# Kernel optimization log

Measured on AMD Instinct MI355X. Metric: run time of the kernel, lower is better.

Reference implementation:

```python
import jax, jax.numpy as jnp
import numpy as np

B, T, VT, E, D = 128, 512, 2048, 1024, 1024  # batch, num_topics, topic_vocab, enc_hid, dec_hid


def setup_inputs() -> dict:
    key = jax.random.key(0)
    ks = jax.random.split(key, 8)
    # Split the Linear weight (in = dec_hid + topic_vocab + enc_hid, concat order: hidden, topic, enc)
    # into per-input blocks; math is identical to Linear(cat([h, t, e])).
    s = 1.0 / np.sqrt(D + VT + E)
    return {
        "hidden": jax.random.normal(ks[0], (B, D), jnp.float32),
        "topic_dict": jax.random.uniform(ks[1], (T, VT), jnp.float32),
        "enc_hidden": jax.random.normal(ks[2], (B, E), jnp.float32),
        "W_h": jax.random.uniform(ks[3], (D, D), jnp.float32, -s, s),
        "W_t": jax.random.uniform(ks[4], (VT, D), jnp.float32, -s, s),
        "W_e": jax.random.uniform(ks[5], (E, D), jnp.float32, -s, s),
        "b": jax.random.uniform(ks[6], (D,), jnp.float32, -s, s),
        "v": jax.random.uniform(ks[7], (D,), jnp.float32),
    }


def reference(hidden, topic_dict, enc_hidden, W_h, W_t, W_e, b, v):
    # Decompose Linear(cat(h, t, e)) = h@W_h + t@W_t + e@W_e + b; avoids the
    # repeated/concatenated [B, T, D+VT+E] buffer while computing the same math.
    h_proj = hidden @ W_h          # [B, D]
    t_proj = topic_dict @ W_t      # [T, D]
    e_proj = enc_hidden @ W_e      # [B, D]
    energy = jnp.tanh(h_proj[:, None, :] + e_proj[:, None, :] + t_proj[None, :, :] + b)  # [B, T, D]
    score = jnp.einsum("btd,d->bt", energy, v)  # [B, T]
    return jax.nn.softmax(score, axis=1)[:, None, :]  # [B, 1, T]
```

## Files before the change

### kernel.cpp

```cpp
#include <hip/hip_runtime.h>
#include <hip/hip_fp16.h>

#define B_ 128
#define T_ 512
#define VT_ 2048
#define E_ 1024
#define D_ 1024

typedef _Float16 h8 __attribute__((ext_vector_type(8)));
typedef float f4 __attribute__((ext_vector_type(4)));

#define C2LE 2.8853900817779268f
#define L2E  1.4426950408889634f

static __device__ __forceinline__ float rcpf(float x) { return __builtin_amdgcn_rcpf(x); }
static __device__ __forceinline__ float ex2(float x)  { return __builtin_amdgcn_exp2f(x); }

#define P_FLOATS   (4 * 640 * 1024)
#define SP_FLOATS  (8 * 128 * 512)
#define PA_HALVES  (640 * 2048)
#define PB_WH      0
#define PB_WE      1048576
#define PB_WT      2097152

__device__ __forceinline__ void packA_do(const float* __restrict__ src, int ld, int KBs,
                                         _Float16* __restrict__ dst, int mb_off, int kb_off, int t)
{
    const int lane = t & 63;
    const int fb = t >> 6;
    const int kb = fb % KBs, mb = fb / KBs;
    const int r = lane & 15, g = lane >> 4;
    const float* s = src + (size_t)(mb * 16 + r) * ld + kb * 32 + g * 8;
    f4 v0 = *(const f4*)s, v1 = *(const f4*)(s + 4);
    h8 h;
    h[0] = (_Float16)v0[0]; h[1] = (_Float16)v0[1]; h[2] = (_Float16)v0[2]; h[3] = (_Float16)v0[3];
    h[4] = (_Float16)v1[0]; h[5] = (_Float16)v1[1]; h[6] = (_Float16)v1[2]; h[7] = (_Float16)v1[3];
    *(h8*)(dst + ((size_t)((mb_off + mb) * 64 + (kb_off + kb)) * 64 + lane) * 8) = h;
}

__device__ __forceinline__ void packB_do(const float* __restrict__ W, int KB,
                                         _Float16* __restrict__ dst, int t)
{
    const int lane = t & 63;
    const int fb = t >> 6;
    const int kb = fb % KB, nb = fb / KB;
    const int r = lane & 15, g = lane >> 4;
    const float* s = W + (size_t)(kb * 32 + g * 8) * 1024 + nb * 16 + r;
    h8 h;
    #pragma unroll
    for (int j = 0; j < 8; ++j) h[j] = (_Float16)s[(size_t)j * 1024];
    *(h8*)(dst + ((size_t)(nb * KB + kb) * 64 + lane) * 8) = h;
}

__global__ __launch_bounds__(256) void pack_kernel(
    const float* __restrict__ hidden, const float* __restrict__ topic,
    const float* __restrict__ enc,
    const float* __restrict__ W_h, const float* __restrict__ W_t, const float* __restrict__ W_e,
    _Float16* __restrict__ pA, _Float16* __restrict__ pB)
{
    const int bid = blockIdx.x, tid = threadIdx.x;
    if      (bid <   64) packA_do(hidden, 1024, 32, pA, 0,  0, bid * 256 + tid);
    else if (bid <  128) packA_do(enc,    1024, 32, pA, 0, 32, (bid -  64) * 256 + tid);
    else if (bid <  640) packA_do(topic,  2048, 64, pA, 8,  0, (bid - 128) * 256 + tid);
    else if (bid < 1152) packB_do(W_h, 32, pB + PB_WH, (bid -  640) * 256 + tid);
    else if (bid < 1664) packB_do(W_e, 32, pB + PB_WE, (bid - 1152) * 256 + tid);
    else                 packB_do(W_t, 64, pB + PB_WT, (bid - 1664) * 256 + tid);
}

__global__ __launch_bounds__(256) void gemm_kernel(const _Float16* __restrict__ pA,
                                                   const _Float16* __restrict__ pB,
                                                   float* __restrict__ P)
{
    const int mt = blockIdx.x, nt = blockIdx.y, s = blockIdx.z;
    const int tid = threadIdx.x, wave = tid >> 6, lane = tid & 63;
    const int wm = (wave >> 1) * 32, wn = (wave & 1) * 32;
    const int r = lane & 15, g = lane >> 4;

    const int kb0 = s * 16;
    const int mb0 = (mt * 64 + wm) >> 4;
    const int nb0 = (nt * 64 + wn) >> 4;

    const _Float16* Bp; int KB_B, kbB;
    if (mt < 2) {
        if (kb0 < 32) { Bp = pB + PB_WH; kbB = kb0; }
        else          { Bp = pB + PB_WE; kbB = kb0 - 32; }
        KB_B = 32;
    } else {
        Bp = pB + PB_WT; kbB = kb0; KB_B = 64;
    }

    const _Float16* Ap = pA + ((size_t)(mb0 * 64 + kb0) * 64 + lane) * 8;
    const _Float16* Bq = Bp + ((size_t)(nb0 * KB_B + kbB) * 64 + lane) * 8;
    const size_t aStrI = (size_t)64 * 512;
    const size_t bStrJ = (size_t)KB_B * 512;

    f4 acc00{}, acc01{}, acc10{}, acc11{};
    #pragma unroll 4
    for (int ks = 0; ks < 16; ++ks) {
        h8 a0 = *(const h8*)(Ap);
        h8 a1 = *(const h8*)(Ap + aStrI);
        h8 b0 = *(const h8*)(Bq);
        h8 b1 = *(const h8*)(Bq + bStrJ);
        acc00 = __builtin_amdgcn_mfma_f32_16x16x32_f16(a0, b0, acc00, 0, 0, 0);
        acc01 = __builtin_amdgcn_mfma_f32_16x16x32_f16(a0, b1, acc01, 0, 0, 0);
        acc10 = __builtin_amdgcn_mfma_f32_16x16x32_f16(a1, b0, acc10, 0, 0, 0);
        acc11 = __builtin_amdgcn_mfma_f32_16x16x32_f16(a1, b1, acc11, 0, 0, 0);
        Ap += 512; Bq += 512;
    }

    float* Pp = P + ((size_t)s * 640 + mt * 64 + wm + g * 4) * 1024 + nt * 64 + wn + r;
    #pragma unroll
    for (int q = 0; q < 4; ++q) {
        Pp[(size_t)q * 1024 +  0]        = C2LE * acc00[q];
        Pp[(size_t)q * 1024 + 16]        = C2LE * acc01[q];
        Pp[(size_t)(16 + q) * 1024 +  0] = C2LE * acc10[q];
        Pp[(size_t)(16 + q) * 1024 + 16] = C2LE * acc11[q];
    }
}

__global__ __launch_bounds__(256) void score_kernel(const float* __restrict__ P,
                                                    const float* __restrict__ bias,
                                                    const float* __restrict__ v,
                                                    float* __restrict__ SP)
{
    __shared__ float Xs[16][128];
    __shared__ float Ys[64][128];
    __shared__ float vs[128];

    const int tid = threadIdx.x;
    const int b0 = blockIdx.x * 16;
    const int t0 = blockIdx.y * 64;
    const int d0 = blockIdx.z * 128;
    const size_t PS = (size_t)640 * 1024;

    #pragma unroll
    for (int i = 0; i < 8; ++i) {
        int idx = tid + i * 256;
        int row = idx >> 5, c4 = idx & 31;
        size_t off = (size_t)(128 + t0 + row) * 1024 + d0 + c4 * 4;
        f4 vv = *(const f4*)&P[off];
        vv += *(const f4*)&P[off + PS];
        vv += *(const f4*)&P[off + 2 * PS];
        vv += *(const f4*)&P[off + 3 * PS];
        *(f4*)&Ys[row][(c4 ^ (row & 15)) * 4] = vv;
    }
    #pragma unroll
    for (int i = 0; i < 2; ++i) {
        int idx = tid + i * 256;
        int row = idx >> 5, c4 = idx & 31;
        size_t off = (size_t)(b0 + row) * 1024 + d0 + c4 * 4;
        f4 vv = *(const f4*)&P[off];
        vv += *(const f4*)&P[off + PS];
        vv += *(const f4*)&P[off + 2 * PS];
        vv += *(const f4*)&P[off + 3 * PS];
        f4 bb = *(const f4*)&bias[d0 + c4 * 4];
        vv += bb * C2LE;
        *(f4*)&Xs[row][(c4 ^ (row & 15)) * 4] = vv;
    }
    if (tid < 32) *(f4*)&vs[tid * 4] = *(const f4*)&v[d0 + tid * 4];
    __syncthreads();

    const int tq = tid & 31, bq = tid >> 5;
    const int sx0 = bq & 15, sx1 = (bq + 8) & 15, sy = tq & 15;
    float a00 = 0.f, a01 = 0.f, a10 = 0.f, a11 = 0.f;

    for (int dd = 0; dd < 32; ++dd) {
        f4 xa = *(const f4*)&Xs[bq]     [(dd ^ sx0) * 4];
        f4 xb = *(const f4*)&Xs[bq + 8] [(dd ^ sx1) * 4];
        f4 ya = *(const f4*)&Ys[tq]     [(dd ^ sy) * 4];
        f4 yb = *(const f4*)&Ys[tq + 32][(dd ^ sy) * 4];
        f4 vv = *(const f4*)&vs[dd * 4];
        #pragma unroll
        for (int j = 0; j < 4; ++j) {
            float e;
            e = ex2(xa[j] + ya[j]); a00 += vv[j] * rcpf(e + 1.0f);
            e = ex2(xa[j] + yb[j]); a01 += vv[j] * rcpf(e + 1.0f);
            e = ex2(xb[j] + ya[j]); a10 += vv[j] * rcpf(e + 1.0f);
            e = ex2(xb[j] + yb[j]); a11 += vv[j] * rcpf(e + 1.0f);
        }
    }

    float* sp = SP + (size_t)blockIdx.z * (B_ * T_);
    sp[(size_t)(b0 + bq)     * T_ + t0 + tq]      = a00;
    sp[(size_t)(b0 + bq)     * T_ + t0 + tq + 32] = a01;
    sp[(size_t)(b0 + bq + 8) * T_ + t0 + tq]      = a10;
    sp[(size_t)(b0 + bq + 8) * T_ + t0 + tq + 32] = a11;
}

__global__ __launch_bounds__(256) void softmax_kernel(
    const float* __restrict__ SP, float* __restrict__ out)
{
    const int b = blockIdx.x, tid = threadIdx.x;
    float s0 = 0.f, s1 = 0.f;
    #pragma unroll
    for (int z = 0; z < 8; ++z) {
        s0 += SP[(size_t)z * B_ * T_ + (size_t)b * T_ + tid];
        s1 += SP[(size_t)z * B_ * T_ + (size_t)b * T_ + tid + 256];
    }
    s0 *= -2.0f; s1 *= -2.0f;

    float m = fmaxf(s0, s1);
    #pragma unroll
    for (int off = 32; off >= 1; off >>= 1) m = fmaxf(m, __shfl_xor(m, off));
    __shared__ float red[4];
    __shared__ float red2[4];
    const int wv = tid >> 6;
    if ((tid & 63) == 0) red[wv] = m;
    __syncthreads();
    m = fmaxf(fmaxf(red[0], red[1]), fmaxf(red[2], red[3]));

    float e0 = ex2((s0 - m) * L2E);
    float e1 = ex2((s1 - m) * L2E);
    float sum = e0 + e1;
    #pragma unroll
    for (int off = 32; off >= 1; off >>= 1) sum += __shfl_xor(sum, off);
    if ((tid & 63) == 0) red2[wv] = sum;
    __syncthreads();
    sum = red2[0] + red2[1] + red2[2] + red2[3];

    const float rs = rcpf(sum);
    out[(size_t)b * T_ + tid]       = e0 * rs;
    out[(size_t)b * T_ + tid + 256] = e1 * rs;
}

extern "C" void kernel_launch(void* const* d_in, const int* in_sizes, int n_in,
                              void* d_out, int out_size, void* d_ws, size_t ws_size,
                              hipStream_t stream)
{
    const float* hidden = (const float*)d_in[0];
    const float* topic  = (const float*)d_in[1];
    const float* enc    = (const float*)d_in[2];
    const float* W_h    = (const float*)d_in[3];
    const float* W_t    = (const float*)d_in[4];
    const float* W_e    = (const float*)d_in[5];
    const float* bvec   = (const float*)d_in[6];
    const float* vvec   = (const float*)d_in[7];
    float* out = (float*)d_out;

    float* P      = (float*)d_ws;
    float* SPb    = P + P_FLOATS;
    _Float16* pA  = (_Float16*)(SPb + SP_FLOATS);
    _Float16* pB  = pA + PA_HALVES;

    pack_kernel<<<2688, 256, 0, stream>>>(hidden, topic, enc, W_h, W_t, W_e, pA, pB);
    gemm_kernel<<<dim3(10, 16, 4), 256, 0, stream>>>(pA, pB, P);
    score_kernel<<<dim3(8, 8, 8), 256, 0, stream>>>(P, bvec, vvec, SPb);
    softmax_kernel<<<128, 256, 0, stream>>>(SPb, out);
}
```

Before: 119.6 us.

## Widen GEMM N-tile, double split-K, add separate partial-sum reduce kernel

The GEMM tile grows from 64x64 to 64x128 per block (each wave computes a 32x64 block with 8 MFMA accumulators), split-K goes from 4 to 8 slices, and a swizzled 1D grid of 640 blocks is used. A new reduce kernel sums the 8 partial slices and adds the bias once, so the score kernel reads a single reduced buffer instead of re-summing partials in every block. This is meant to raise operand reuse and parallelism and to remove redundant partial-sum reads in the score stage. The cost is an extra kernel launch and twice as much partial-sum traffic written and read through memory.

Result: faster. 115.0 us (-3.8%).

```diff
diff --git a/kernel.cpp b/kernel.cpp
--- a/kernel.cpp
+++ b/kernel.cpp
@@ -16,7 +16,8 @@
 static __device__ __forceinline__ float rcpf(float x) { return __builtin_amdgcn_rcpf(x); }
 static __device__ __forceinline__ float ex2(float x)  { return __builtin_amdgcn_exp2f(x); }
 
-#define P_FLOATS   (4 * 640 * 1024)
+#define P_FLOATS   (8 * 640 * 1024)
+#define R_FLOATS   (640 * 1024)
 #define SP_FLOATS  (8 * 128 * 512)
 #define PA_HALVES  (640 * 2048)
 #define PB_WH      0
@@ -67,59 +68,85 @@
     else                 packB_do(W_t, 64, pB + PB_WT, (bid - 1664) * 256 + tid);
 }
 
-__global__ __launch_bounds__(256) void gemm_kernel(const _Float16* __restrict__ pA,
-                                                   const _Float16* __restrict__ pB,
-                                                   float* __restrict__ P)
-{
-    const int mt = blockIdx.x, nt = blockIdx.y, s = blockIdx.z;
+__global__ __launch_bounds__(256, 3) void gemm_kernel(const _Float16* __restrict__ pA,
+                                                      const _Float16* __restrict__ pB,
+                                                      float* __restrict__ P)
+{
+    const int lin = blockIdx.x;
+    const int sw  = (lin & 7) * 80 + (lin >> 3);
+    const int s   = sw / 80;
+    const int rem = sw % 80;
+    const int mt  = rem % 10;
+    const int nt  = rem / 10;
+
     const int tid = threadIdx.x, wave = tid >> 6, lane = tid & 63;
-    const int wm = (wave >> 1) * 32, wn = (wave & 1) * 32;
+    const int wm = (wave >> 1) * 32;
+    const int wn = (wave & 1) * 64;
     const int r = lane & 15, g = lane >> 4;
 
-    const int kb0 = s * 16;
-    const int mb0 = (mt * 64 + wm) >> 4;
-    const int nb0 = (nt * 64 + wn) >> 4;
-
-    const _Float16* Bp; int KB_B, kbB;
+    const int mb0 = mt * 4 + (wm >> 4);
+    const int nb0 = (nt * 128 + wn) >> 4;
+    const int kb0 = s * 8;
+
+    const _Float16* Bp; int KB_B, kbB0;
     if (mt < 2) {
-        if (kb0 < 32) { Bp = pB + PB_WH; kbB = kb0; }
-        else          { Bp = pB + PB_WE; kbB = kb0 - 32; }
+        if (kb0 < 32) { Bp = pB + PB_WH; kbB0 = kb0; }
+        else          { Bp = pB + PB_WE; kbB0 = kb0 - 32; }
         KB_B = 32;
-    } else {
-        Bp = pB + PB_WT; kbB = kb0; KB_B = 64;
-    }
+    } else { Bp = pB + PB_WT; kbB0 = kb0; KB_B = 64; }
 
     const _Float16* Ap = pA + ((size_t)(mb0 * 64 + kb0) * 64 + lane) * 8;
-    const _Float16* Bq = Bp + ((size_t)(nb0 * KB_B + kbB) * 64 + lane) * 8;
-    const size_t aStrI = (size_t)64 * 512;
-    const size_t bStrJ = (size_t)KB_B * 512;
-
-    f4 acc00{}, acc01{}, acc10{}, acc11{};
-    #pragma unroll 4
-    for (int ks = 0; ks < 16; ++ks) {
-        h8 a0 = *(const h8*)(Ap);
-        h8 a1 = *(const h8*)(Ap + aStrI);
-        h8 b0 = *(const h8*)(Bq);
-        h8 b1 = *(const h8*)(Bq + bStrJ);
-        acc00 = __builtin_amdgcn_mfma_f32_16x16x32_f16(a0, b0, acc00, 0, 0, 0);
-        acc01 = __builtin_amdgcn_mfma_f32_16x16x32_f16(a0, b1, acc01, 0, 0, 0);
-        acc10 = __builtin_amdgcn_mfma_f32_16x16x32_f16(a1, b0, acc10, 0, 0, 0);
-        acc11 = __builtin_amdgcn_mfma_f32_16x16x32_f16(a1, b1, acc11, 0, 0, 0);
-        Ap += 512; Bq += 512;
-    }
-
-    float* Pp = P + ((size_t)s * 640 + mt * 64 + wm + g * 4) * 1024 + nt * 64 + wn + r;
-    #pragma unroll
-    for (int q = 0; q < 4; ++q) {
-        Pp[(size_t)q * 1024 +  0]        = C2LE * acc00[q];
-        Pp[(size_t)q * 1024 + 16]        = C2LE * acc01[q];
-        Pp[(size_t)(16 + q) * 1024 +  0] = C2LE * acc10[q];
-        Pp[(size_t)(16 + q) * 1024 + 16] = C2LE * acc11[q];
-    }
-}
-
-__global__ __launch_bounds__(256) void score_kernel(const float* __restrict__ P,
-                                                    const float* __restrict__ bias,
+    const _Float16* Bq = Bp + ((size_t)(nb0 * KB_B + kbB0) * 64 + lane) * 8;
+    const size_t aStrM = (size_t)64 * 512;
+    const size_t bStrN = (size_t)KB_B * 512;
+
+    f4 acc[2][4] = {};
+    #pragma unroll
+    for (int ks = 0; ks < 8; ++ks) {
+        h8 a0 = *(const h8*)(Ap + (size_t)ks * 512);
+        h8 a1 = *(const h8*)(Ap + aStrM + (size_t)ks * 512);
+        h8 b0 = *(const h8*)(Bq + (size_t)ks * 512);
+        h8 b1 = *(const h8*)(Bq + bStrN + (size_t)ks * 512);
+        h8 b2 = *(const h8*)(Bq + 2 * bStrN + (size_t)ks * 512);
+        h8 b3 = *(const h8*)(Bq + 3 * bStrN + (size_t)ks * 512);
+        acc[0][0] = __builtin_amdgcn_mfma_f32_16x16x32_f16(a0, b0, acc[0][0], 0, 0, 0);
+        acc[0][1] = __builtin_amdgcn_mfma_f32_16x16x32_f16(a0, b1, acc[0][1], 0, 0, 0);
+        acc[0][2] = __builtin_amdgcn_mfma_f32_16x16x32_f16(a0, b2, acc[0][2], 0, 0, 0);
+        acc[0][3] = __builtin_amdgcn_mfma_f32_16x16x32_f16(a0, b3, acc[0][3], 0, 0, 0);
+        acc[1][0] = __builtin_amdgcn_mfma_f32_16x16x32_f16(a1, b0, acc[1][0], 0, 0, 0);
+        acc[1][1] = __builtin_amdgcn_mfma_f32_16x16x32_f16(a1, b1, acc[1][1], 0, 0, 0);
+        acc[1][2] = __builtin_amdgcn_mfma_f32_16x16x32_f16(a1, b2, acc[1][2], 0, 0, 0);
+        acc[1][3] = __builtin_amdgcn_mfma_f32_16x16x32_f16(a1, b3, acc[1][3], 0, 0, 0);
+    }
+
+    float* Pp = P + ((size_t)s * 640 + mt * 64 + wm + g * 4) * 1024 + nt * 128 + wn + r;
+    #pragma unroll
+    for (int i = 0; i < 2; ++i)
+        #pragma unroll
+        for (int j = 0; j < 4; ++j)
+            #pragma unroll
+            for (int q = 0; q < 4; ++q)
+                Pp[(size_t)(i * 16 + q) * 1024 + j * 16] = C2LE * acc[i][j][q];
+}
+
+__global__ __launch_bounds__(256) void reduce_kernel(const float* __restrict__ P,
+                                                     const float* __restrict__ bias,
+                                                     float* __restrict__ R)
+{
+    const int row = blockIdx.x, tid = threadIdx.x;
+    const size_t off = (size_t)row * 1024 + tid * 4;
+    const size_t PS = (size_t)640 * 1024;
+    f4 acc = *(const f4*)&P[off];
+    #pragma unroll
+    for (int z = 1; z < 8; ++z) acc += *(const f4*)&P[off + (size_t)z * PS];
+    if (row < 128) {
+        f4 bb = *(const f4*)&bias[tid * 4];
+        acc += bb * C2LE;
+    }
+    *(f4*)&R[off] = acc;
+}
+
+__global__ __launch_bounds__(256) void score_kernel(const float* __restrict__ R,
                                                     const float* __restrict__ v,
                                                     float* __restrict__ SP)
 {
@@ -131,30 +158,19 @@
     const int b0 = blockIdx.x * 16;
     const int t0 = blockIdx.y * 64;
     const int d0 = blockIdx.z * 128;
-    const size_t PS = (size_t)640 * 1024;
 
     #pragma unroll
     for (int i = 0; i < 8; ++i) {
         int idx = tid + i * 256;
         int row = idx >> 5, c4 = idx & 31;
-        size_t off = (size_t)(128 + t0 + row) * 1024 + d0 + c4 * 4;
-        f4 vv = *(const f4*)&P[off];
-        vv += *(const f4*)&P[off + PS];
-        vv += *(const f4*)&P[off + 2 * PS];
-        vv += *(const f4*)&P[off + 3 * PS];
+        f4 vv = *(const f4*)&R[(size_t)(128 + t0 + row) * 1024 + d0 + c4 * 4];
         *(f4*)&Ys[row][(c4 ^ (row & 15)) * 4] = vv;
     }
     #pragma unroll
     for (int i = 0; i < 2; ++i) {
         int idx = tid + i * 256;
         int row = idx >> 5, c4 = idx & 31;
-        size_t off = (size_t)(b0 + row) * 1024 + d0 + c4 * 4;
-        f4 vv = *(const f4*)&P[off];
-        vv += *(const f4*)&P[off + PS];
-        vv += *(const f4*)&P[off + 2 * PS];
-        vv += *(const f4*)&P[off + 3 * PS];
-        f4 bb = *(const f4*)&bias[d0 + c4 * 4];
-        vv += bb * C2LE;
+        f4 vv = *(const f4*)&R[(size_t)(b0 + row) * 1024 + d0 + c4 * 4];
         *(f4*)&Xs[row][(c4 ^ (row & 15)) * 4] = vv;
     }
     if (tid < 32) *(f4*)&vs[tid * 4] = *(const f4*)&v[d0 + tid * 4];
@@ -238,12 +254,14 @@
     float* out = (float*)d_out;
 
     float* P      = (float*)d_ws;
-    float* SPb    = P + P_FLOATS;
+    float* R      = P + P_FLOATS;
+    float* SPb    = R + R_FLOATS;
     _Float16* pA  = (_Float16*)(SPb + SP_FLOATS);
     _Float16* pB  = pA + PA_HALVES;
 
     pack_kernel<<<2688, 256, 0, stream>>>(hidden, topic, enc, W_h, W_t, W_e, pA, pB);
-    gemm_kernel<<<dim3(10, 16, 4), 256, 0, stream>>>(pA, pB, P);
-    score_kernel<<<dim3(8, 8, 8), 256, 0, stream>>>(P, bvec, vvec, SPb);
+    gemm_kernel<<<640, 256, 0, stream>>>(pA, pB, P);
+    reduce_kernel<<<640, 256, 0, stream>>>(P, bvec, R);
+    score_kernel<<<dim3(8, 8, 8), 256, 0, stream>>>(R, vvec, SPb);
     softmax_kernel<<<128, 256, 0, stream>>>(SPb, out);
 }
```
